# Performance work log

Hardware: AMD Instinct MI355X
Metric: run time of the kernel (lower is better)

Reference implementation:

```python
import jax, jax.numpy as jnp
import numpy as np

NUM_EMBEDDINGS = 1024  # K
EMBEDDING_DIM = 64     # D
COMMITMENT_COST = 0.25


def setup_inputs() -> dict:
    key = jax.random.key(0)
    k1, k2 = jax.random.split(key)
    inputs = jax.random.normal(k1, (16, 4096, EMBEDDING_DIM), dtype=jnp.float32)
    # codebook init: uniform(-1/K, 1/K) as in nn.Embedding init in the module
    embedding = jax.random.uniform(
        k2, (NUM_EMBEDDINGS, EMBEDDING_DIM), dtype=jnp.float32,
        minval=-1.0 / NUM_EMBEDDINGS, maxval=1.0 / NUM_EMBEDDINGS)
    return {"inputs": inputs, "embedding": embedding}


def reference(inputs, embedding):
    input_shape = inputs.shape
    K = embedding.shape[0]
    flat = inputs.reshape(-1, embedding.shape[1])  # [N, D]

    distances = (jnp.sum(flat * flat, axis=1, keepdims=True)
                 + jnp.sum(embedding * embedding, axis=1)
                 - 2.0 * jnp.einsum('nd,kd->nk', flat, embedding))
    idx = jnp.argmin(distances, axis=1)                      # [N]
    encodings = jax.nn.one_hot(idx, K, dtype=flat.dtype)     # [N, K]
    quantized = embedding[idx]                               # [N, D] gather

    codebook_loss = jnp.mean((jax.lax.stop_gradient(quantized) - flat) ** 2)
    commitment_loss = jnp.mean((quantized - jax.lax.stop_gradient(flat)) ** 2)
    loss = codebook_loss + COMMITMENT_COST * commitment_loss

    # straight-through estimator
    quantized_st = flat + jax.lax.stop_gradient(quantized - flat)

    quantized_st = quantized_st.reshape(input_shape)
    encodings = encodings.reshape(*input_shape[:-1], K)
    return (quantized_st, encodings, loss, codebook_loss, commitment_loss)
```

## Files before the change

kernel.cpp:

```cpp
#include <hip/hip_runtime.h>
#include <float.h>

#define NVEC 65536
#define KCB  1024
#define DIM  64
#define ENC_OFF   ((size_t)NVEC * DIM)
#define LOSS_OFF  (ENC_OFF + (size_t)NVEC * KCB)
#define BAND 6e-5f

#define WS_SE_BOFF   64
#define WS_LIST_BOFF 4160
#define LIST_CAP     49152
#define WS_EH_BOFF   (WS_LIST_BOFF + LIST_CAP * 4)
#define WS_EL_BOFF   (WS_EH_BOFF + 131072)

typedef __attribute__((ext_vector_type(8))) short short8;
typedef __attribute__((ext_vector_type(4))) float f32x4;
typedef __attribute__((ext_vector_type(4))) unsigned int u32x4;

__device__ __forceinline__ unsigned short f2bf(float f) {
    unsigned u = __float_as_uint(f);
    return (unsigned short)((u + 0x7FFFu + ((u >> 16) & 1u)) >> 16);
}
__device__ __forceinline__ float bf2f(unsigned short h) {
    return __uint_as_float((unsigned)h << 16);
}

__global__ __launch_bounds__(256) void vq_prep(const float* __restrict__ emb,
                                               float* __restrict__ se,
                                               int* __restrict__ counter,
                                               unsigned short* __restrict__ eh,
                                               unsigned short* __restrict__ el,
                                               float* __restrict__ loss3) {
    int g = blockIdx.x * 256 + threadIdx.x;
    if (g == 0) *counter = 0;
    if (g < 3) loss3[g] = 0.0f;
    {
        const f32x4* er = (const f32x4*)(emb + (size_t)g * DIM);
        double s0 = 0.0, s1 = 0.0, s2 = 0.0, s3 = 0.0;
#pragma unroll
        for (int i = 0; i < 16; i++) {
            f32x4 e = er[i];
            s0 = fma((double)e.x, (double)e.x, s0);
            s1 = fma((double)e.y, (double)e.y, s1);
            s2 = fma((double)e.z, (double)e.z, s2);
            s3 = fma((double)e.w, (double)e.w, s3);
        }
        se[g] = (float)((s0 + s1) + (s2 + s3));
    }
    for (int i = g; i < KCB * DIM; i += 1024) {
        float v = emb[i];
        unsigned short h = f2bf(v);
        eh[i] = h;
        el[i] = f2bf(v - bf2f(h));
    }
}

__global__ __launch_bounds__(256) void vq_screen(const float* __restrict__ x,
                                                 const float* __restrict__ emb,
                                                 const float* __restrict__ se,
                                                 const unsigned short* __restrict__ eh,
                                                 const unsigned short* __restrict__ el,
                                                 int* __restrict__ counter,
                                                 unsigned* __restrict__ list,
                                                 float* __restrict__ outq,
                                                 float* __restrict__ enc,
                                                 float* __restrict__ lossacc) {
    __shared__ unsigned short sEh[256 * 72];
    __shared__ unsigned short sEl[256 * 72];
    __shared__ float sse[KCB];
    __shared__ int sidx[64];
    __shared__ float red[4];

    const int tid = threadIdx.x;
    const int wave = tid >> 6, lane = tid & 63;
    const int q = lane >> 4, c = lane & 15;

    for (int t = tid; t < KCB; t += 256) sse[t] = se[t];

    const int vecm = blockIdx.x * 64 + wave * 16 + c;
    float xa[16];
    {
        const f32x4* xp = (const f32x4*)(x + (size_t)vecm * DIM);
        ((f32x4*)xa)[0] = xp[2 * q];
        ((f32x4*)xa)[1] = xp[2 * q + 1];
        ((f32x4*)xa)[2] = xp[8 + 2 * q];
        ((f32x4*)xa)[3] = xp[8 + 2 * q + 1];
    }
    short8 ah0, al0, ah1, al1;
#pragma unroll
    for (int j = 0; j < 8; j++) {
        unsigned short h0 = f2bf(xa[j]);
        ah0[j] = (short)h0;
        al0[j] = (short)f2bf(xa[j] - bf2f(h0));
        unsigned short h1 = f2bf(xa[8 + j]);
        ah1[j] = (short)h1;
        al1[j] = (short)f2bf(xa[8 + j] - bf2f(h1));
    }

    float b1[4], b2[4];
    int i1[4];
#pragma unroll
    for (int r = 0; r < 4; r++) { b1[r] = FLT_MAX; b2[r] = FLT_MAX; i1[r] = 0; }

    for (int st = 0; st < 4; st++) {
        __syncthreads();
        for (int u = tid; u < 4096; u += 256) {
            int arr = u >> 11;
            int v = u & 2047;
            int code = v >> 3, unit = v & 7;
            const u32x4* src = (const u32x4*)((arr ? el : eh)
                                + ((size_t)(st * 256 + code) * 64 + unit * 8));
            u32x4 val = *src;
            unsigned short* dst = (arr ? sEl : sEh) + (code * 72 + unit * 8);
            *(u32x4*)dst = val;
        }
        __syncthreads();

#pragma unroll 2
        for (int t = 0; t < 16; t++) {
            int cl = t * 16 + c;
            const unsigned short* bph = sEh + (cl * 72 + q * 8);
            const unsigned short* bpl = sEl + (cl * 72 + q * 8);
            short8 bh0 = *(const short8*)bph;
            short8 bh1 = *(const short8*)(bph + 32);
            short8 bl0 = *(const short8*)bpl;
            short8 bl1 = *(const short8*)(bpl + 32);
            f32x4 acc = {0.f, 0.f, 0.f, 0.f};
            acc = __builtin_amdgcn_mfma_f32_16x16x32_bf16(ah0, bh0, acc, 0, 0, 0);
            acc = __builtin_amdgcn_mfma_f32_16x16x32_bf16(ah1, bh1, acc, 0, 0, 0);
            acc = __builtin_amdgcn_mfma_f32_16x16x32_bf16(ah0, bl0, acc, 0, 0, 0);
            acc = __builtin_amdgcn_mfma_f32_16x16x32_bf16(ah1, bl1, acc, 0, 0, 0);
            acc = __builtin_amdgcn_mfma_f32_16x16x32_bf16(al0, bh0, acc, 0, 0, 0);
            acc = __builtin_amdgcn_mfma_f32_16x16x32_bf16(al1, bh1, acc, 0, 0, 0);
            int kcur = st * 256 + t * 16 + c;
            float sek = sse[kcur];
#pragma unroll
            for (int r = 0; r < 4; r++) {
                float v = fmaf(-2.f, acc[r], sek);
                bool lt = v < b1[r];
                b2[r] = fminf(fmaxf(v, b1[r]), b2[r]);
                b1[r] = lt ? v : b1[r];
                i1[r] = lt ? kcur : i1[r];
            }
        }
    }

#pragma unroll
    for (int m = 1; m <= 8; m <<= 1) {
#pragma unroll
        for (int r = 0; r < 4; r++) {
            float ob1 = __shfl_xor(b1[r], m, 64);
            float ob2 = __shfl_xor(b2[r], m, 64);
            int oi = __shfl_xor(i1[r], m, 64);
            float nb2 = fminf(fmaxf(b1[r], ob1), fminf(b2[r], ob2));
            if (ob1 < b1[r]) { b1[r] = ob1; i1[r] = oi; }
            b2[r] = nb2;
        }
    }

    if (c == 0) {
#pragma unroll
        for (int r = 0; r < 4; r++) {
            int row = wave * 16 + q * 4 + r;
            sidx[row] = i1[r];
            if (b2[r] - b1[r] < BAND) {
                int pos = atomicAdd(counter, 1);
                if (pos < LIST_CAP)
                    list[pos] = (unsigned)(blockIdx.x * 64 + row) | ((unsigned)i1[r] << 16);
            }
        }
    }
    __syncthreads();

    {
        int vec = tid >> 2, ch = tid & 3;
        int id = sidx[vec];
        const f32x4* ebp = (const f32x4*)(emb + (size_t)id * DIM) + ch * 4;
        const f32x4* xp = (const f32x4*)(x + (size_t)(blockIdx.x * 64 + vec) * DIM) + ch * 4;
        f32x4* op = (f32x4*)(outq + (size_t)(blockIdx.x * 64 + vec) * DIM) + ch * 4;
        float sq = 0.0f;
#pragma unroll
        for (int i = 0; i < 4; i++) {
            f32x4 e = ebp[i];
            f32x4 xv = xp[i];
            f32x4 d = e - xv;
            sq += d.x * d.x + d.y * d.y + d.z * d.z + d.w * d.w;
            op[i] = e;
        }
        for (int off = 32; off; off >>= 1) sq += __shfl_down(sq, off);
        if ((tid & 63) == 0) red[tid >> 6] = sq;
        __syncthreads();
        if (tid == 0) atomicAdd(lossacc, red[0] + red[1] + red[2] + red[3]);
    }

    f32x4* encb = (f32x4*)enc + (size_t)blockIdx.x * 64 * 256;
    for (int t = tid; t < 64 * 256; t += 256) {
        int id = sidx[t >> 8];
        int j = (t & 255) << 2;
        f32x4 v;
        v.x = (id == j + 0) ? 1.0f : 0.0f;
        v.y = (id == j + 1) ? 1.0f : 0.0f;
        v.z = (id == j + 2) ? 1.0f : 0.0f;
        v.w = (id == j + 3) ? 1.0f : 0.0f;
        encb[t] = v;
    }
}

__global__ __launch_bounds__(256) void vq_refine(const float* __restrict__ x,
                                                 const float* __restrict__ emb,
                                                 const float* __restrict__ se,
                                                 const int* __restrict__ counter,
                                                 const unsigned* __restrict__ list,
                                                 float* __restrict__ outq,
                                                 float* __restrict__ enc,
                                                 float* __restrict__ lossacc) {
    const int cnt = min(*counter, LIST_CAP);
    const int lane = threadIdx.x & 63;
    const int gw = blockIdx.x * 4 + (threadIdx.x >> 6);
    const int nw = gridDim.x * 4;

    for (int it = gw; it < cnt; it += nw) {
        unsigned ent = list[it];
        int n = (int)(ent & 0xFFFFu);
        int oldi = (int)(ent >> 16);

        const float4* xr = (const float4*)(x + (size_t)n * DIM);
        float xf[64];
#pragma unroll
        for (int i = 0; i < 16; i++) ((float4*)xf)[i] = xr[i];

        float r[8];
#pragma unroll
        for (int j = 0; j < 8; j++) r[j] = __fmul_rn(xf[j], xf[j]);
#pragma unroll
        for (int b = 1; b < 8; b++)
#pragma unroll
            for (int j = 0; j < 8; j++)
                r[j] = __fadd_rn(r[j], __fmul_rn(xf[8 * b + j], xf[8 * b + j]));
        float sx = __fadd_rn(
            __fadd_rn(__fadd_rn(r[0], r[1]), __fadd_rn(r[2], r[3])),
            __fadd_rn(__fadd_rn(r[4], r[5]), __fadd_rn(r[6], r[7])));

        float bd = 3.4e38f;
        int bk = lane * 16;
        for (int cc = 0; cc < 16; cc++) {
            int k = lane * 16 + cc;
            const float4* er = (const float4*)(emb + (size_t)k * DIM);
            double s0 = 0.0, s1 = 0.0, s2 = 0.0, s3 = 0.0;
#pragma unroll
            for (int i = 0; i < 16; i++) {
                float4 e = er[i];
                s0 = fma((double)e.x, (double)xf[4 * i + 0], s0);
                s1 = fma((double)e.y, (double)xf[4 * i + 1], s1);
                s2 = fma((double)e.z, (double)xf[4 * i + 2], s2);
                s3 = fma((double)e.w, (double)xf[4 * i + 3], s3);
            }
            float dot32 = (float)((s0 + s1) + (s2 + s3));
            float t1 = __fadd_rn(sx, se[k]);
            float d = __fsub_rn(t1, __fmul_rn(2.0f, dot32));
            if (d < bd) { bd = d; bk = k; }
        }
        for (int off = 32; off; off >>= 1) {
            float od = __shfl_down(bd, off);
            int ok = __shfl_down(bk, off);
            if (od < bd || (od == bd && ok < bk)) { bd = od; bk = ok; }
        }
        if (lane == 0 && bk != oldi) {
            enc[(size_t)n * KCB + oldi] = 0.0f;
            enc[(size_t)n * KCB + bk] = 1.0f;
            const float4* en = (const float4*)(emb + (size_t)bk * DIM);
            const float4* eo = (const float4*)(emb + (size_t)oldi * DIM);
            float4* oq = (float4*)(outq + (size_t)n * DIM);
            float dsq = 0.0f;
#pragma unroll
            for (int i = 0; i < 16; i++) {
                float4 a = en[i], b = eo[i];
                float4 xv = ((float4*)xf)[i];
                float n0 = a.x - xv.x, n1 = a.y - xv.y, n2 = a.z - xv.z, n3 = a.w - xv.w;
                float o0 = b.x - xv.x, o1 = b.y - xv.y, o2 = b.z - xv.z, o3 = b.w - xv.w;
                dsq += (n0 * n0 + n1 * n1 + n2 * n2 + n3 * n3)
                     - (o0 * o0 + o1 * o1 + o2 * o2 + o3 * o3);
                oq[i] = a;
            }
            atomicAdd(lossacc, dsq);
        }
    }
}

__global__ void vq_fin(float* __restrict__ loss3) {
    if (threadIdx.x == 0 && blockIdx.x == 0) {
        float m = loss3[1] * (1.0f / (float)((size_t)NVEC * DIM));
        loss3[0] = 1.25f * m;
        loss3[1] = m;
        loss3[2] = m;
    }
}

extern "C" void kernel_launch(void* const* d_in, const int* in_sizes, int n_in,
                              void* d_out, int out_size, void* d_ws, size_t ws_size,
                              hipStream_t stream) {
    const float* x = (const float*)d_in[0];
    const float* emb = (const float*)d_in[1];
    float* out = (float*)d_out;
    int* counter = (int*)d_ws;
    float* se = (float*)((char*)d_ws + WS_SE_BOFF);
    unsigned* list = (unsigned*)((char*)d_ws + WS_LIST_BOFF);
    unsigned short* eh = (unsigned short*)((char*)d_ws + WS_EH_BOFF);
    unsigned short* el = (unsigned short*)((char*)d_ws + WS_EL_BOFF);

    hipLaunchKernelGGL(vq_prep, dim3(4), dim3(256), 0, stream,
                       emb, se, counter, eh, el, out + LOSS_OFF);
    hipLaunchKernelGGL(vq_screen, dim3(NVEC / 64), dim3(256), 0, stream,
                       x, emb, se, eh, el, counter, list,
                       out, out + ENC_OFF, out + LOSS_OFF + 1);
    hipLaunchKernelGGL(vq_refine, dim3(1024), dim3(256), 0, stream,
                       x, emb, se, counter, list,
                       out, out + ENC_OFF, out + LOSS_OFF + 1);
    hipLaunchKernelGGL(vq_fin, dim3(1), dim3(64), 0, stream, out + LOSS_OFF);
}
```

Baseline: 440.0 us.

## Fuse refine pass into main kernel and read codebook directly from global/L2

Merges the separate screen and refine kernels into one kernel. Ambiguous rows are now flagged in shared memory and recomputed in fp64 inside the same block, before the quantized and one-hot outputs are written. This removes the global atomic list, the extra launch, and the scattered fix-up writes to the one-hot output. It also drops the LDS staging of the bf16 hi/lo codebook in favour of direct global/L2 loads, widens the prep kernel grid, and uses nontemporal stores for the large output writes. The risks are that blocks with many ambiguous rows become stragglers, and that the direct codebook loads may be slower than LDS reuse.

```diff
diff --git a/kernel.cpp b/kernel.cpp
--- a/kernel.cpp
+++ b/kernel.cpp
@@ -8,11 +8,9 @@
 #define LOSS_OFF  (ENC_OFF + (size_t)NVEC * KCB)
 #define BAND 6e-5f
 
-#define WS_SE_BOFF   64
-#define WS_LIST_BOFF 4160
-#define LIST_CAP     49152
-#define WS_EH_BOFF   (WS_LIST_BOFF + LIST_CAP * 4)
-#define WS_EL_BOFF   (WS_EH_BOFF + 131072)
+#define WS_SE_BOFF 64
+#define WS_EH_BOFF 8192
+#define WS_EL_BOFF (8192 + 131072)
 
 typedef __attribute__((ext_vector_type(8))) short short8;
 typedef __attribute__((ext_vector_type(4))) float f32x4;
@@ -28,14 +26,12 @@
 
 __global__ __launch_bounds__(256) void vq_prep(const float* __restrict__ emb,
                                                float* __restrict__ se,
-                                               int* __restrict__ counter,
                                                unsigned short* __restrict__ eh,
                                                unsigned short* __restrict__ el,
                                                float* __restrict__ loss3) {
     int g = blockIdx.x * 256 + threadIdx.x;
-    if (g == 0) *counter = 0;
     if (g < 3) loss3[g] = 0.0f;
-    {
+    if (g < KCB) {
         const f32x4* er = (const f32x4*)(emb + (size_t)g * DIM);
         double s0 = 0.0, s1 = 0.0, s2 = 0.0, s3 = 0.0;
 #pragma unroll
@@ -48,7 +44,7 @@
         }
         se[g] = (float)((s0 + s1) + (s2 + s3));
     }
-    for (int i = g; i < KCB * DIM; i += 1024) {
+    for (int i = g; i < KCB * DIM; i += 64 * 256) {
         float v = emb[i];
         unsigned short h = f2bf(v);
         eh[i] = h;
@@ -56,26 +52,26 @@
     }
 }
 
-__global__ __launch_bounds__(256) void vq_screen(const float* __restrict__ x,
-                                                 const float* __restrict__ emb,
-                                                 const float* __restrict__ se,
-                                                 const unsigned short* __restrict__ eh,
-                                                 const unsigned short* __restrict__ el,
-                                                 int* __restrict__ counter,
-                                                 unsigned* __restrict__ list,
-                                                 float* __restrict__ outq,
-                                                 float* __restrict__ enc,
-                                                 float* __restrict__ lossacc) {
-    __shared__ unsigned short sEh[256 * 72];
-    __shared__ unsigned short sEl[256 * 72];
+__global__ __launch_bounds__(256) void vq_main(const float* __restrict__ x,
+                                               const float* __restrict__ emb,
+                                               const float* __restrict__ se,
+                                               const unsigned short* __restrict__ eh,
+                                               const unsigned short* __restrict__ el,
+                                               float* __restrict__ outq,
+                                               float* __restrict__ enc,
+                                               float* __restrict__ lossacc) {
     __shared__ float sse[KCB];
-    __shared__ int sidx[64];
+    __shared__ int   sidx[64];
+    __shared__ int   sflag[64];
+    __shared__ int   scnt;
     __shared__ float red[4];
+    __shared__ float sxrow[4][64];
 
     const int tid = threadIdx.x;
     const int wave = tid >> 6, lane = tid & 63;
     const int q = lane >> 4, c = lane & 15;
 
+    if (tid == 0) scnt = 0;
     for (int t = tid; t < KCB; t += 256) sse[t] = se[t];
 
     const int vecm = blockIdx.x * 64 + wave * 16 + c;
@@ -97,52 +93,37 @@
         ah1[j] = (short)h1;
         al1[j] = (short)f2bf(xa[8 + j] - bf2f(h1));
     }
+    __syncthreads();
 
     float b1[4], b2[4];
     int i1[4];
 #pragma unroll
     for (int r = 0; r < 4; r++) { b1[r] = FLT_MAX; b2[r] = FLT_MAX; i1[r] = 0; }
 
-    for (int st = 0; st < 4; st++) {
-        __syncthreads();
-        for (int u = tid; u < 4096; u += 256) {
-            int arr = u >> 11;
-            int v = u & 2047;
-            int code = v >> 3, unit = v & 7;
-            const u32x4* src = (const u32x4*)((arr ? el : eh)
-                                + ((size_t)(st * 256 + code) * 64 + unit * 8));
-            u32x4 val = *src;
-            unsigned short* dst = (arr ? sEl : sEh) + (code * 72 + unit * 8);
-            *(u32x4*)dst = val;
-        }
-        __syncthreads();
-
 #pragma unroll 2
-        for (int t = 0; t < 16; t++) {
-            int cl = t * 16 + c;
-            const unsigned short* bph = sEh + (cl * 72 + q * 8);
-            const unsigned short* bpl = sEl + (cl * 72 + q * 8);
-            short8 bh0 = *(const short8*)bph;
-            short8 bh1 = *(const short8*)(bph + 32);
-            short8 bl0 = *(const short8*)bpl;
-            short8 bl1 = *(const short8*)(bpl + 32);
-            f32x4 acc = {0.f, 0.f, 0.f, 0.f};
-            acc = __builtin_amdgcn_mfma_f32_16x16x32_bf16(ah0, bh0, acc, 0, 0, 0);
-            acc = __builtin_amdgcn_mfma_f32_16x16x32_bf16(ah1, bh1, acc, 0, 0, 0);
-            acc = __builtin_amdgcn_mfma_f32_16x16x32_bf16(ah0, bl0, acc, 0, 0, 0);
-            acc = __builtin_amdgcn_mfma_f32_16x16x32_bf16(ah1, bl1, acc, 0, 0, 0);
-            acc = __builtin_amdgcn_mfma_f32_16x16x32_bf16(al0, bh0, acc, 0, 0, 0);
-            acc = __builtin_amdgcn_mfma_f32_16x16x32_bf16(al1, bh1, acc, 0, 0, 0);
-            int kcur = st * 256 + t * 16 + c;
-            float sek = sse[kcur];
-#pragma unroll
-            for (int r = 0; r < 4; r++) {
-                float v = fmaf(-2.f, acc[r], sek);
-                bool lt = v < b1[r];
-                b2[r] = fminf(fmaxf(v, b1[r]), b2[r]);
-                b1[r] = lt ? v : b1[r];
-                i1[r] = lt ? kcur : i1[r];
-            }
+    for (int t = 0; t < 64; t++) {
+        int kcur = t * 16 + c;
+        const unsigned short* bph = eh + ((size_t)kcur << 6) + q * 8;
+        const unsigned short* bpl = el + ((size_t)kcur << 6) + q * 8;
+        short8 bh0 = *(const short8*)bph;
+        short8 bh1 = *(const short8*)(bph + 32);
+        short8 bl0 = *(const short8*)bpl;
+        short8 bl1 = *(const short8*)(bpl + 32);
+        f32x4 acc = {0.f, 0.f, 0.f, 0.f};
+        acc = __builtin_amdgcn_mfma_f32_16x16x32_bf16(ah0, bh0, acc, 0, 0, 0);
+        acc = __builtin_amdgcn_mfma_f32_16x16x32_bf16(ah1, bh1, acc, 0, 0, 0);
+        acc = __builtin_amdgcn_mfma_f32_16x16x32_bf16(ah0, bl0, acc, 0, 0, 0);
+        acc = __builtin_amdgcn_mfma_f32_16x16x32_bf16(ah1, bl1, acc, 0, 0, 0);
+        acc = __builtin_amdgcn_mfma_f32_16x16x32_bf16(al0, bh0, acc, 0, 0, 0);
+        acc = __builtin_amdgcn_mfma_f32_16x16x32_bf16(al1, bh1, acc, 0, 0, 0);
+        float sek = sse[kcur];
+#pragma unroll
+        for (int r = 0; r < 4; r++) {
+            float v = fmaf(-2.f, acc[r], sek);
+            bool lt = v < b1[r];
+            b2[r] = fminf(fmaxf(v, b1[r]), b2[r]);
+            b1[r] = lt ? v : b1[r];
+            i1[r] = lt ? kcur : i1[r];
         }
     }
 
@@ -158,18 +139,65 @@
             b2[r] = nb2;
         }
     }
-
     if (c == 0) {
 #pragma unroll
         for (int r = 0; r < 4; r++) {
             int row = wave * 16 + q * 4 + r;
             sidx[row] = i1[r];
             if (b2[r] - b1[r] < BAND) {
-                int pos = atomicAdd(counter, 1);
-                if (pos < LIST_CAP)
-                    list[pos] = (unsigned)(blockIdx.x * 64 + row) | ((unsigned)i1[r] << 16);
+                int p = atomicAdd(&scnt, 1);
+                sflag[p] = row;
             }
         }
+    }
+    __syncthreads();
+
+    int cnt = scnt;
+    for (int f = wave; f < cnt; f += 4) {
+        int row = sflag[f];
+        int n = blockIdx.x * 64 + row;
+        if (lane < 16)
+            ((f32x4*)sxrow[wave])[lane] = ((const f32x4*)(x + (size_t)n * DIM))[lane];
+        const float* xr = sxrow[wave];
+
+        float r8[8];
+#pragma unroll
+        for (int j = 0; j < 8; j++) r8[j] = 0.0f;
+#pragma unroll
+        for (int b = 0; b < 8; b++)
+#pragma unroll
+            for (int j = 0; j < 8; j++)
+                r8[j] = __fadd_rn(r8[j], __fmul_rn(xr[8 * b + j], xr[8 * b + j]));
+        float sx = __fadd_rn(
+            __fadd_rn(__fadd_rn(r8[0], r8[1]), __fadd_rn(r8[2], r8[3])),
+            __fadd_rn(__fadd_rn(r8[4], r8[5]), __fadd_rn(r8[6], r8[7])));
+
+        float bd = FLT_MAX;
+        int bk = lane * 16;
+        for (int cc = 0; cc < 16; cc++) {
+            int k = lane * 16 + cc;
+            const f32x4* er = (const f32x4*)(emb + (size_t)k * DIM);
+            double s0 = 0.0, s1 = 0.0, s2 = 0.0, s3 = 0.0;
+#pragma unroll
+            for (int i = 0; i < 16; i++) {
+                f32x4 e = er[i];
+                f32x4 xv = ((const f32x4*)xr)[i];
+                s0 = fma((double)e.x, (double)xv.x, s0);
+                s1 = fma((double)e.y, (double)xv.y, s1);
+                s2 = fma((double)e.z, (double)xv.z, s2);
+                s3 = fma((double)e.w, (double)xv.w, s3);
+            }
+            float dot32 = (float)((s0 + s1) + (s2 + s3));
+            float t1 = __fadd_rn(sx, sse[k]);
+            float d = __fsub_rn(t1, __fmul_rn(2.0f, dot32));
+            if (d < bd) { bd = d; bk = k; }
+        }
+        for (int off = 32; off; off >>= 1) {
+            float od = __shfl_down(bd, off);
+            int ok = __shfl_down(bk, off);
+            if (od < bd || (od == bd && ok < bk)) { bd = od; bk = ok; }
+        }
+        if (lane == 0) sidx[row] = bk;
     }
     __syncthreads();
 
@@ -186,7 +214,7 @@
             f32x4 xv = xp[i];
             f32x4 d = e - xv;
             sq += d.x * d.x + d.y * d.y + d.z * d.z + d.w * d.w;
-            op[i] = e;
+            __builtin_nontemporal_store(e, op + i);
         }
         for (int off = 32; off; off >>= 1) sq += __shfl_down(sq, off);
         if ((tid & 63) == 0) red[tid >> 6] = sq;
@@ -203,88 +231,7 @@
         v.y = (id == j + 1) ? 1.0f : 0.0f;
         v.z = (id == j + 2) ? 1.0f : 0.0f;
         v.w = (id == j + 3) ? 1.0f : 0.0f;
-        encb[t] = v;
-    }
-}
-
-__global__ __launch_bounds__(256) void vq_refine(const float* __restrict__ x,
-                                                 const float* __restrict__ emb,
-                                                 const float* __restrict__ se,
-                                                 const int* __restrict__ counter,
-                                                 const unsigned* __restrict__ list,
-                                                 float* __restrict__ outq,
-                                                 float* __restrict__ enc,
-                                                 float* __restrict__ lossacc) {
-    const int cnt = min(*counter, LIST_CAP);
-    const int lane = threadIdx.x & 63;
-    const int gw = blockIdx.x * 4 + (threadIdx.x >> 6);
-    const int nw = gridDim.x * 4;
-
-    for (int it = gw; it < cnt; it += nw) {
-        unsigned ent = list[it];
-        int n = (int)(ent & 0xFFFFu);
-        int oldi = (int)(ent >> 16);
-
-        const float4* xr = (const float4*)(x + (size_t)n * DIM);
-        float xf[64];
-#pragma unroll
-        for (int i = 0; i < 16; i++) ((float4*)xf)[i] = xr[i];
-
-        float r[8];
-#pragma unroll
-        for (int j = 0; j < 8; j++) r[j] = __fmul_rn(xf[j], xf[j]);
-#pragma unroll
-        for (int b = 1; b < 8; b++)
-#pragma unroll
-            for (int j = 0; j < 8; j++)
-                r[j] = __fadd_rn(r[j], __fmul_rn(xf[8 * b + j], xf[8 * b + j]));
-        float sx = __fadd_rn(
-            __fadd_rn(__fadd_rn(r[0], r[1]), __fadd_rn(r[2], r[3])),
-            __fadd_rn(__fadd_rn(r[4], r[5]), __fadd_rn(r[6], r[7])));
-
-        float bd = 3.4e38f;
-        int bk = lane * 16;
-        for (int cc = 0; cc < 16; cc++) {
-            int k = lane * 16 + cc;
-            const float4* er = (const float4*)(emb + (size_t)k * DIM);
-            double s0 = 0.0, s1 = 0.0, s2 = 0.0, s3 = 0.0;
-#pragma unroll
-            for (int i = 0; i < 16; i++) {
-                float4 e = er[i];
-                s0 = fma((double)e.x, (double)xf[4 * i + 0], s0);
-                s1 = fma((double)e.y, (double)xf[4 * i + 1], s1);
-                s2 = fma((double)e.z, (double)xf[4 * i + 2], s2);
-                s3 = fma((double)e.w, (double)xf[4 * i + 3], s3);
-            }
-            float dot32 = (float)((s0 + s1) + (s2 + s3));
-            float t1 = __fadd_rn(sx, se[k]);
-            float d = __fsub_rn(t1, __fmul_rn(2.0f, dot32));
-            if (d < bd) { bd = d; bk = k; }
-        }
-        for (int off = 32; off; off >>= 1) {
-            float od = __shfl_down(bd, off);
-            int ok = __shfl_down(bk, off);
-            if (od < bd || (od == bd && ok < bk)) { bd = od; bk = ok; }
-        }
-        if (lane == 0 && bk != oldi) {
-            enc[(size_t)n * KCB + oldi] = 0.0f;
-            enc[(size_t)n * KCB + bk] = 1.0f;
-            const float4* en = (const float4*)(emb + (size_t)bk * DIM);
-            const float4* eo = (const float4*)(emb + (size_t)oldi * DIM);
-            float4* oq = (float4*)(outq + (size_t)n * DIM);
-            float dsq = 0.0f;
-#pragma unroll
-            for (int i = 0; i < 16; i++) {
-                float4 a = en[i], b = eo[i];
-                float4 xv = ((float4*)xf)[i];
-                float n0 = a.x - xv.x, n1 = a.y - xv.y, n2 = a.z - xv.z, n3 = a.w - xv.w;
-                float o0 = b.x - xv.x, o1 = b.y - xv.y, o2 = b.z - xv.z, o3 = b.w - xv.w;
-                dsq += (n0 * n0 + n1 * n1 + n2 * n2 + n3 * n3)
-                     - (o0 * o0 + o1 * o1 + o2 * o2 + o3 * o3);
-                oq[i] = a;
-            }
-            atomicAdd(lossacc, dsq);
-        }
+        __builtin_nontemporal_store(v, encb + t);
     }
 }
 
@@ -303,19 +250,13 @@
     const float* x = (const float*)d_in[0];
     const float* emb = (const float*)d_in[1];
     float* out = (float*)d_out;
-    int* counter = (int*)d_ws;
     float* se = (float*)((char*)d_ws + WS_SE_BOFF);
-    unsigned* list = (unsigned*)((char*)d_ws + WS_LIST_BOFF);
     unsigned short* eh = (unsigned short*)((char*)d_ws + WS_EH_BOFF);
     unsigned short* el = (unsigned short*)((char*)d_ws + WS_EL_BOFF);
 
-    hipLaunchKernelGGL(vq_prep, dim3(4), dim3(256), 0, stream,
-                       emb, se, counter, eh, el, out + LOSS_OFF);
-    hipLaunchKernelGGL(vq_screen, dim3(NVEC / 64), dim3(256), 0, stream,
-                       x, emb, se, eh, el, counter, list,
-                       out, out + ENC_OFF, out + LOSS_OFF + 1);
-    hipLaunchKernelGGL(vq_refine, dim3(1024), dim3(256), 0, stream,
-                       x, emb, se, counter, list,
-                       out, out + ENC_OFF, out + LOSS_OFF + 1);
+    hipLaunchKernelGGL(vq_prep, dim3(64), dim3(256), 0, stream,
+                       emb, se, eh, el, out + LOSS_OFF);
+    hipLaunchKernelGGL(vq_main, dim3(NVEC / 64), dim3(256), 0, stream,
+                       x, emb, se, eh, el, out, out + ENC_OFF, out + LOSS_OFF + 1);
     hipLaunchKernelGGL(vq_fin, dim3(1), dim3(64), 0, stream, out + LOSS_OFF);
 }
```

Result: slower. 484.4 us (+10.1%).
